# Kernel tuning notes

Hardware: AMD Instinct MI355X
Metric: run time of the kernel (lower is better)

Reference implementation:

```python
import jax, jax.numpy as jnp
import numpy as np
from math import factorial

D = 2          # qudit dimension
L = 13         # number of qudits: state dim = D**L = 8192
J, K = 0, 1    # levels coupled by the gate
CUTOFF = 10    # Taylor truncation order
INDEX = set(range(13))


def _series(z, parity):
    # sum_{i=1..CUTOFF, i%2==parity} z**i / i!   (truncated exp split into even/odd parts)
    s = jnp.zeros((), dtype=jnp.complex64)
    for i in range(1, CUTOFF + 1):
        if i % 2 == parity:
            s = s + z ** i / factorial(i)
    return s


def _gate(theta):
    # single-qudit RX gate matrix, truncated-Taylor version matching the torch code
    z = (-0.5j) * theta.astype(jnp.complex64)
    odd = _series(z, 1)   # ~ -i sin(theta/2)
    even = _series(z, 0)  # ~ cos(theta/2) - 1
    M = jnp.eye(D, dtype=jnp.complex64)
    M = M.at[J, K].add(odd)
    M = M.at[K, J].add(odd)
    M = M.at[J, J].add(even)
    M = M.at[K, K].add(even)
    return M


def setup_inputs() -> dict:
    key = jax.random.key(0)
    k1, k2, k3 = jax.random.split(key, 3)
    dim = D ** L
    return {
        "x_real": jax.random.normal(k1, (dim, 64), dtype=jnp.float32),
        "x_imag": jax.random.normal(k2, (dim, 64), dtype=jnp.float32),
        "angle": jax.random.normal(k3, (L,), dtype=jnp.float32),
    }


def reference(x_real, x_imag, angle):
    x = x_real.astype(jnp.complex64) + 1j * x_imag.astype(jnp.complex64)
    eye = jnp.eye(D, dtype=jnp.complex64)
    U = jnp.eye(1, dtype=jnp.complex64)
    for i in range(L):  # fixed structural loop over qudits (13 iterations)
        M = _gate(angle[i]) if i in INDEX else eye
        U = jnp.kron(U, M)
    out = U @ x  # [D^L, B] complex64
    return jnp.stack([out.real, out.imag])  # [2, D^L, B] float32
```

## Files before the change

kernel.cpp:

```cpp
#include <hip/hip_runtime.h>

#define PLANE (8192 * 64)

typedef float f4 __attribute__((ext_vector_type(4)));

__device__ __forceinline__ void gate_coeffs(float theta, float& a, float& s) {
    float t = 0.5f * theta;
    float u = t * t;
    s = t * (1.f + u * (-1.f/6.f + u * (1.f/120.f + u * (-1.f/5040.f + u * (1.f/362880.f)))));
    a = 1.f + u * (-0.5f + u * (1.f/24.f + u * (-1.f/720.f + u * (1.f/40320.f + u * (-1.f/3628800.f)))));
}

__device__ __forceinline__ void bf(f4& v0, f4& v1, float a, float s) {
    f4 n0, n1;
    n0.x = a * v0.x + s * v1.y;  n0.y = a * v0.y - s * v1.x;
    n0.z = a * v0.z + s * v1.w;  n0.w = a * v0.w - s * v1.z;
    n1.x = a * v1.x + s * v0.y;  n1.y = a * v1.y - s * v0.x;
    n1.z = a * v1.z + s * v0.w;  n1.w = a * v1.w - s * v0.z;
    v0 = n0; v1 = n1;
}

__device__ __forceinline__ int slotA(int row, int c) {
    return row * 8 + (c ^ (row & 7));
}
__device__ __forceinline__ int sB(int h, int c) {
    return ((h >> 1) << 3) | (((((h & 1) << 2) | c) ^ (h >> 1)) & 7);
}

__global__ __launch_bounds__(256) void rx_low(const float* __restrict__ xr,
                                              const float* __restrict__ xi,
                                              const float* __restrict__ angle,
                                              f4* __restrict__ ws4) {
    __shared__ f4 la[512];
    const int t = threadIdx.x, bid = blockIdx.x;
    const int g = bid >> 2, qa = bid & 3;

    {
        const int row = t >> 2, c4 = t & 3;
        const f4* xr4 = (const f4*)xr;
        const f4* xi4 = (const f4*)xi;
        int ga = (g * 64 + row) * 16 + qa * 4 + c4;
        f4 re = xr4[ga], im = xi4[ga];
        la[slotA(row, 2 * c4)]     = (f4){re.x, im.x, re.y, im.y};
        la[slotA(row, 2 * c4 + 1)] = (f4){re.z, im.z, re.w, im.w};
    }
    __syncthreads();

    const int cp8 = t & 7, rp = t >> 3;
    #pragma unroll
    for (int b = 0; b <= 4; ++b) {
        float a, s; gate_coeffs(angle[12 - b], a, s);
        int lo = ((rp >> b) << (b + 1)) | (rp & ((1 << b) - 1));
        int i0 = slotA(lo, cp8), i1 = slotA(lo + (1 << b), cp8);
        f4 v0 = la[i0], v1 = la[i1];
        bf(v0, v1, a, s);
        la[i0] = v0; la[i1] = v1;
        __syncthreads();
    }

    float a5, s5; gate_coeffs(angle[7], a5, s5);
    f4 v0 = la[slotA(rp, cp8)], v1 = la[slotA(rp + 32, cp8)];
    bf(v0, v1, a5, s5);
    const int oct = qa * 2 + (cp8 >> 2), c = cp8 & 3;
    const int e = sB(g, c);
    ws4[(size_t)(rp * 8 + oct) * 512 + e]        = v0;
    ws4[(size_t)((rp + 32) * 8 + oct) * 512 + e] = v1;
}

__global__ __launch_bounds__(256) void rx_high(const float* __restrict__ angle,
                                               const f4* __restrict__ ws4,
                                               float* __restrict__ out) {
    __shared__ f4 lb[512];
    const int t = threadIdx.x, bid = blockIdx.x;
    const int m = bid >> 3, oct = bid & 7;

    {
        const int hh = t >> 2, cL = t & 3;
        const f4* src = ws4 + (size_t)bid * 512;
        f4 w0 = src[sB(hh, cL)];
        f4 w1 = src[sB(hh + 64, cL)];
        float a6, s6; gate_coeffs(angle[0], a6, s6);
        bf(w0, w1, a6, s6);
        lb[sB(hh, cL)]      = w0;
        lb[sB(hh + 64, cL)] = w1;
    }
    __syncthreads();

    {
        const int hp = t & 63, cL = t >> 6;
        float a, s; gate_coeffs(angle[6], a, s);
        int i0 = sB(2 * hp, cL), i1 = sB(2 * hp + 1, cL);
        f4 v0 = lb[i0], v1 = lb[i1];
        bf(v0, v1, a, s);
        lb[i0] = v0; lb[i1] = v1;
    }
    __syncthreads();

    const int cB = t & 3, hp = t >> 2;
    #pragma unroll
    for (int q = 1; q <= 4; ++q) {
        float a, s; gate_coeffs(angle[6 - q], a, s);
        int h0 = ((hp >> q) << (q + 1)) | (hp & ((1 << q) - 1));
        int i0 = sB(h0, cB), i1 = sB(h0 + (1 << q), cB);
        f4 v0 = lb[i0], v1 = lb[i1];
        bf(v0, v1, a, s);
        lb[i0] = v0; lb[i1] = v1;
        __syncthreads();
    }

    float a5, s5; gate_coeffs(angle[1], a5, s5);
    const int h0f = ((hp >> 5) << 6) | (hp & 31);
    f4 v0 = lb[sB(h0f, cB)], v1 = lb[sB(h0f + 32, cB)];
    bf(v0, v1, a5, s5);
    float2* outre2 = (float2*)out;
    float2* outim2 = (float2*)(out + PLANE);
    const int CP = oct * 4 + cB;
    const int r0 = h0f * 64 + m;
    outre2[r0 * 32 + CP]          = make_float2(v0.x, v0.z);
    outim2[r0 * 32 + CP]          = make_float2(v0.y, v0.w);
    outre2[(r0 + 2048) * 32 + CP] = make_float2(v1.x, v1.z);
    outim2[(r0 + 2048) * 32 + CP] = make_float2(v1.y, v1.w);
}

extern "C" void kernel_launch(void* const* d_in, const int* in_sizes, int n_in,
                              void* d_out, int out_size, void* d_ws, size_t ws_size,
                              hipStream_t stream) {
    const float* xr    = (const float*)d_in[0];
    const float* xi    = (const float*)d_in[1];
    const float* angle = (const float*)d_in[2];
    float* out = (float*)d_out;
    f4*    ws4 = (f4*)d_ws;

    rx_low <<<512, 256, 0, stream>>>(xr, xi, angle, ws4);
    rx_high<<<512, 256, 0, stream>>>(angle, ws4, out);
}
```

Measured before the change: 14.73 us.

## Apply two butterfly stages per LDS pass and double per-block tile size

```diff
diff --git a/kernel.cpp b/kernel.cpp
--- a/kernel.cpp
+++ b/kernel.cpp
@@ -20,106 +20,134 @@
     v0 = n0; v1 = n1;
 }
 
-__device__ __forceinline__ int slotA(int row, int c) {
-    return row * 8 + (c ^ (row & 7));
-}
-__device__ __forceinline__ int sB(int h, int c) {
-    return ((h >> 1) << 3) | (((((h & 1) << 2) | c) ^ (h >> 1)) & 7);
-}
-
 __global__ __launch_bounds__(256) void rx_low(const float* __restrict__ xr,
                                               const float* __restrict__ xi,
                                               const float* __restrict__ angle,
                                               f4* __restrict__ ws4) {
-    __shared__ f4 la[512];
+    __shared__ f4 l4[64 * 16];
     const int t = threadIdx.x, bid = blockIdx.x;
-    const int g = bid >> 2, qa = bid & 3;
+    const int g = bid >> 1, half = bid & 1;
+    const int cp = t & 15, rq = t >> 4;
+
+    const float2* xr2 = (const float2*)xr;
+    const float2* xi2 = (const float2*)xi;
 
     {
-        const int row = t >> 2, c4 = t & 3;
-        const f4* xr4 = (const f4*)xr;
-        const f4* xi4 = (const f4*)xi;
-        int ga = (g * 64 + row) * 16 + qa * 4 + c4;
-        f4 re = xr4[ga], im = xi4[ga];
-        la[slotA(row, 2 * c4)]     = (f4){re.x, im.x, re.y, im.y};
-        la[slotA(row, 2 * c4 + 1)] = (f4){re.z, im.z, re.w, im.w};
+        float a0, s0, a1, s1;
+        gate_coeffs(angle[12], a0, s0);
+        gate_coeffs(angle[11], a1, s1);
+        f4 v[4];
+        #pragma unroll
+        for (int k = 0; k < 4; ++k) {
+            int gi = (g * 64 + 4 * rq + k) * 32 + half * 16 + cp;
+            float2 re = xr2[gi], im = xi2[gi];
+            v[k] = (f4){re.x, im.x, re.y, im.y};
+        }
+        bf(v[0], v[1], a0, s0); bf(v[2], v[3], a0, s0);
+        bf(v[0], v[2], a1, s1); bf(v[1], v[3], a1, s1);
+        #pragma unroll
+        for (int k = 0; k < 4; ++k) l4[(4 * rq + k) * 16 + cp] = v[k];
     }
     __syncthreads();
 
-    const int cp8 = t & 7, rp = t >> 3;
-    #pragma unroll
-    for (int b = 0; b <= 4; ++b) {
-        float a, s; gate_coeffs(angle[12 - b], a, s);
-        int lo = ((rp >> b) << (b + 1)) | (rp & ((1 << b) - 1));
-        int i0 = slotA(lo, cp8), i1 = slotA(lo + (1 << b), cp8);
-        f4 v0 = la[i0], v1 = la[i1];
-        bf(v0, v1, a, s);
-        la[i0] = v0; la[i1] = v1;
-        __syncthreads();
+    {
+        float a2, s2, a3, s3;
+        gate_coeffs(angle[10], a2, s2);
+        gate_coeffs(angle[9],  a3, s3);
+        int base = ((rq >> 2) << 4) | (rq & 3);
+        f4 w0 = l4[(base     ) * 16 + cp], w1 = l4[(base +  4) * 16 + cp];
+        f4 w2 = l4[(base +  8) * 16 + cp], w3 = l4[(base + 12) * 16 + cp];
+        bf(w0, w1, a2, s2); bf(w2, w3, a2, s2);
+        bf(w0, w2, a3, s3); bf(w1, w3, a3, s3);
+        l4[(base     ) * 16 + cp] = w0; l4[(base +  4) * 16 + cp] = w1;
+        l4[(base +  8) * 16 + cp] = w2; l4[(base + 12) * 16 + cp] = w3;
     }
+    __syncthreads();
 
-    float a5, s5; gate_coeffs(angle[7], a5, s5);
-    f4 v0 = la[slotA(rp, cp8)], v1 = la[slotA(rp + 32, cp8)];
-    bf(v0, v1, a5, s5);
-    const int oct = qa * 2 + (cp8 >> 2), c = cp8 & 3;
-    const int e = sB(g, c);
-    ws4[(size_t)(rp * 8 + oct) * 512 + e]        = v0;
-    ws4[(size_t)((rp + 32) * 8 + oct) * 512 + e] = v1;
+    {
+        float a4, s4, a5, s5;
+        gate_coeffs(angle[8], a4, s4);
+        gate_coeffs(angle[7], a5, s5);
+        f4 w0 = l4[(rq     ) * 16 + cp], w1 = l4[(rq + 16) * 16 + cp];
+        f4 w2 = l4[(rq + 32) * 16 + cp], w3 = l4[(rq + 48) * 16 + cp];
+        bf(w0, w1, a4, s4); bf(w2, w3, a4, s4);
+        bf(w0, w2, a5, s5); bf(w1, w3, a5, s5);
+        const int cp32 = half * 16 + cp, q = cp32 >> 3, cb = cp32 & 7;
+        const int e = g * 8 + cb;
+        ws4[(size_t)((rq     ) * 4 + q) * 1024 + e] = w0;
+        ws4[(size_t)((rq + 16) * 4 + q) * 1024 + e] = w1;
+        ws4[(size_t)((rq + 32) * 4 + q) * 1024 + e] = w2;
+        ws4[(size_t)((rq + 48) * 4 + q) * 1024 + e] = w3;
+    }
 }
 
 __global__ __launch_bounds__(256) void rx_high(const float* __restrict__ angle,
                                                const f4* __restrict__ ws4,
                                                float* __restrict__ out) {
-    __shared__ f4 lb[512];
+    __shared__ f4 l4[128 * 8];
     const int t = threadIdx.x, bid = blockIdx.x;
-    const int m = bid >> 3, oct = bid & 7;
+    const int m = bid >> 2, q = bid & 3;
+    const int cp = t & 7, hq = t >> 3;
 
     {
-        const int hh = t >> 2, cL = t & 3;
-        const f4* src = ws4 + (size_t)bid * 512;
-        f4 w0 = src[sB(hh, cL)];
-        f4 w1 = src[sB(hh + 64, cL)];
-        float a6, s6; gate_coeffs(angle[0], a6, s6);
-        bf(w0, w1, a6, s6);
-        lb[sB(hh, cL)]      = w0;
-        lb[sB(hh + 64, cL)] = w1;
+        float a5, s5, a6, s6;
+        gate_coeffs(angle[1], a5, s5);
+        gate_coeffs(angle[0], a6, s6);
+        const f4* src = ws4 + (size_t)(m * 4 + q) * 1024;
+        f4 v0 = src[(hq     ) * 8 + cp], v1 = src[(hq + 32) * 8 + cp];
+        f4 v2 = src[(hq + 64) * 8 + cp], v3 = src[(hq + 96) * 8 + cp];
+        bf(v0, v1, a5, s5); bf(v2, v3, a5, s5);
+        bf(v0, v2, a6, s6); bf(v1, v3, a6, s6);
+        l4[(hq     ) * 8 + cp] = v0; l4[(hq + 32) * 8 + cp] = v1;
+        l4[(hq + 64) * 8 + cp] = v2; l4[(hq + 96) * 8 + cp] = v3;
     }
     __syncthreads();
 
     {
-        const int hp = t & 63, cL = t >> 6;
-        float a, s; gate_coeffs(angle[6], a, s);
-        int i0 = sB(2 * hp, cL), i1 = sB(2 * hp + 1, cL);
-        f4 v0 = lb[i0], v1 = lb[i1];
-        bf(v0, v1, a, s);
-        lb[i0] = v0; lb[i1] = v1;
+        float a3, s3, a4, s4;
+        gate_coeffs(angle[3], a3, s3);
+        gate_coeffs(angle[2], a4, s4);
+        int base = ((hq >> 3) << 5) | (hq & 7);
+        f4 w0 = l4[(base     ) * 8 + cp], w1 = l4[(base +  8) * 8 + cp];
+        f4 w2 = l4[(base + 16) * 8 + cp], w3 = l4[(base + 24) * 8 + cp];
+        bf(w0, w1, a3, s3); bf(w2, w3, a3, s3);
+        bf(w0, w2, a4, s4); bf(w1, w3, a4, s4);
+        l4[(base     ) * 8 + cp] = w0; l4[(base +  8) * 8 + cp] = w1;
+        l4[(base + 16) * 8 + cp] = w2; l4[(base + 24) * 8 + cp] = w3;
     }
     __syncthreads();
 
-    const int cB = t & 3, hp = t >> 2;
-    #pragma unroll
-    for (int q = 1; q <= 4; ++q) {
-        float a, s; gate_coeffs(angle[6 - q], a, s);
-        int h0 = ((hp >> q) << (q + 1)) | (hp & ((1 << q) - 1));
-        int i0 = sB(h0, cB), i1 = sB(h0 + (1 << q), cB);
-        f4 v0 = lb[i0], v1 = lb[i1];
-        bf(v0, v1, a, s);
-        lb[i0] = v0; lb[i1] = v1;
-        __syncthreads();
+    {
+        float a1, s1, a2, s2;
+        gate_coeffs(angle[5], a1, s1);
+        gate_coeffs(angle[4], a2, s2);
+        int b = ((hq >> 1) << 3) | (hq & 1);
+        f4 w0 = l4[(b    ) * 8 + cp], w1 = l4[(b + 2) * 8 + cp];
+        f4 w2 = l4[(b + 4) * 8 + cp], w3 = l4[(b + 6) * 8 + cp];
+        bf(w0, w1, a1, s1); bf(w2, w3, a1, s1);
+        bf(w0, w2, a2, s2); bf(w1, w3, a2, s2);
+        l4[(b    ) * 8 + cp] = w0; l4[(b + 2) * 8 + cp] = w1;
+        l4[(b + 4) * 8 + cp] = w2; l4[(b + 6) * 8 + cp] = w3;
     }
+    __syncthreads();
 
-    float a5, s5; gate_coeffs(angle[1], a5, s5);
-    const int h0f = ((hp >> 5) << 6) | (hp & 31);
-    f4 v0 = lb[sB(h0f, cB)], v1 = lb[sB(h0f + 32, cB)];
-    bf(v0, v1, a5, s5);
-    float2* outre2 = (float2*)out;
-    float2* outim2 = (float2*)(out + PLANE);
-    const int CP = oct * 4 + cB;
-    const int r0 = h0f * 64 + m;
-    outre2[r0 * 32 + CP]          = make_float2(v0.x, v0.z);
-    outim2[r0 * 32 + CP]          = make_float2(v0.y, v0.w);
-    outre2[(r0 + 2048) * 32 + CP] = make_float2(v1.x, v1.z);
-    outim2[(r0 + 2048) * 32 + CP] = make_float2(v1.y, v1.w);
+    {
+        float a0, s0;
+        gate_coeffs(angle[6], a0, s0);
+        float2* outre2 = (float2*)out;
+        float2* outim2 = (float2*)(out + PLANE);
+        #pragma unroll
+        for (int pp = 0; pp < 2; ++pp) {
+            int hp = hq + 32 * pp;
+            f4 w0 = l4[(2 * hp) * 8 + cp], w1 = l4[(2 * hp + 1) * 8 + cp];
+            bf(w0, w1, a0, s0);
+            int o = ((2 * hp) * 64 + m) * 32 + q * 8 + cp;
+            outre2[o] = make_float2(w0.x, w0.z);
+            outim2[o] = make_float2(w0.y, w0.w);
+            outre2[o + 2048] = make_float2(w1.x, w1.z);
+            outim2[o + 2048] = make_float2(w1.y, w1.w);
+        }
+    }
 }
 
 extern "C" void kernel_launch(void* const* d_in, const int* in_sizes, int n_in,
@@ -131,6 +159,6 @@
     float* out = (float*)d_out;
     f4*    ws4 = (f4*)d_ws;
 
-    rx_low <<<512, 256, 0, stream>>>(xr, xi, angle, ws4);
-    rx_high<<<512, 256, 0, stream>>>(angle, ws4, out);
+    rx_low <<<256, 256, 0, stream>>>(xr, xi, angle, ws4);
+    rx_high<<<256, 256, 0, stream>>>(angle, ws4, out);
 }
```

Result: faster. 13.85 us, median of 2 (-6.0%).
